# Kernel tuning notes

Measured on AMD Instinct MI355X. Metric: run time of the kernel, lower is better.

## Reference

```python
import jax, jax.numpy as jnp
import numpy as np

B, S, D, H = 4, 2048, 1024, 16
DEPTH = D // H
NEG = -1000000000.0


def setup_inputs() -> dict:
    key = jax.random.key(0)
    ks = jax.random.split(key, 11)
    scale = 1.0 / np.sqrt(D)
    return {
        "q": jax.random.normal(ks[0], (B, S, D), jnp.float32),
        "k": jax.random.normal(ks[1], (B, S, D), jnp.float32),
        "v": jax.random.normal(ks[2], (B, S, D), jnp.float32),
        "wq_w": jax.random.normal(ks[3], (D, D), jnp.float32) * scale,
        "wq_b": jax.random.normal(ks[4], (D,), jnp.float32) * 0.01,
        "wk_w": jax.random.normal(ks[5], (D, D), jnp.float32) * scale,
        "wk_b": jax.random.normal(ks[6], (D,), jnp.float32) * 0.01,
        "wv_w": jax.random.normal(ks[7], (D, D), jnp.float32) * scale,
        "wv_b": jax.random.normal(ks[8], (D,), jnp.float32) * 0.01,
        "dense_w": jax.random.normal(ks[9], (D, D), jnp.float32) * scale,
        "dense_b": jax.random.normal(ks[10], (D,), jnp.float32) * 0.01,
    }


def _split_heads(x):
    # (B, S, D) -> (B, H, S, depth)
    b, s, _ = x.shape
    return x.reshape(b, s, H, DEPTH).transpose(0, 2, 1, 3)


def reference(q, k, v, wq_w, wq_b, wk_w, wk_b, wv_w, wv_b, dense_w, dense_b):
    b, s, _ = q.shape
    qh = _split_heads(q @ wq_w.T + wq_b)
    kh = _split_heads(k @ wk_w.T + wk_b)
    vh = _split_heads(v @ wv_w.T + wv_b)
    logits = jnp.einsum('bhqd,bhkd->bhqk', qh, kh) / np.sqrt(DEPTH).astype(np.float32)
    # additive causal mask (strict upper triangle = -1e9)
    mask = jnp.where(jnp.triu(jnp.ones((s, s), jnp.float32), k=1) == 1.0, NEG, 0.0)
    logits = logits + mask
    attn = jax.nn.softmax(logits, axis=-1)
    out = jnp.einsum('bhqk,bhkd->bhqd', attn, vh)
    out = out.transpose(0, 2, 1, 3).reshape(b, s, D)
    return out @ dense_w.T + dense_b
```

## Files before the change

kernel.cpp:

```cpp
#include <hip/hip_runtime.h>
#include <hip/hip_bf16.h>


typedef __attribute__((ext_vector_type(8))) short bf16x8;
typedef __attribute__((ext_vector_type(4))) float f32x4;
typedef __attribute__((ext_vector_type(8))) unsigned short u16x8;

#define MFMA16(a, b, c) __builtin_amdgcn_mfma_f32_16x16x32_bf16(a, b, c, 0, 0, 0)

#define GLOAD_LDS16(gp, lp)                                                    \
  __builtin_amdgcn_global_load_lds(                                            \
      (const __attribute__((address_space(1))) void*)(gp),                     \
      (__attribute__((address_space(3))) void*)(lp), 16, 0, 0)

__device__ __forceinline__ unsigned short f2bf(float f) {
  union { float f; unsigned u; } x; x.f = f;
  unsigned u = x.u;
  return (unsigned short)((u + 0x7fffu + ((u >> 16) & 1u)) >> 16);
}

__device__ __forceinline__ unsigned pk2(float a, float b) {
  union { __hip_bfloat162 h; unsigned u; } cv;
  cv.h = __float22bfloat162_rn(float2{a, b});
  return cv.u;
}

__global__ __launch_bounds__(256) void convert_kernel(
    const float* __restrict__ q, const float* __restrict__ k,
    const float* __restrict__ v, const float* __restrict__ wq,
    const float* __restrict__ wk, const float* __restrict__ wv,
    const float* __restrict__ wd, const float* __restrict__ bq,
    const float* __restrict__ bk, const float* __restrict__ bv,
    unsigned short* __restrict__ dst, float* __restrict__ bias_pack) {
  const size_t tid0 = (size_t)blockIdx.x * blockDim.x + threadIdx.x;
  const size_t nthreads = (size_t)gridDim.x * blockDim.x;
  if (tid0 < 3072) {
    bias_pack[tid0] = tid0 < 1024 ? bq[tid0]
                     : (tid0 < 2048 ? bk[tid0 - 1024] : bv[tid0 - 2048]);
  }
  const size_t NQ = 8192ull * 1024;
  const size_t NW = 1024ull * 1024;
  const size_t total_chunks = (3 * NQ + 4 * NW) / 8;
  for (size_t c = tid0; c < total_chunks; c += nthreads) {
    const size_t e = c * 8;
    const float* src;
    if (e < NQ) src = q + e;
    else if (e < 2 * NQ) src = k + (e - NQ);
    else if (e < 3 * NQ) src = v + (e - 2 * NQ);
    else {
      const size_t we = e - 3 * NQ;
      if (we < NW) src = wq + we;
      else if (we < 2 * NW) src = wk + (we - NW);
      else if (we < 3 * NW) src = wv + (we - 2 * NW);
      else src = wd + (we - 3 * NW);
    }
    f32x4 a = *(const f32x4*)(src);
    f32x4 b = *(const f32x4*)(src + 4);
    u16x8 o;
    o[0] = f2bf(a[0]); o[1] = f2bf(a[1]); o[2] = f2bf(a[2]); o[3] = f2bf(a[3]);
    o[4] = f2bf(b[0]); o[5] = f2bf(b[1]); o[6] = f2bf(b[2]); o[7] = f2bf(b[3]);
    *(u16x8*)(dst + e) = o;
  }
}

template <int MODE>
__global__ __launch_bounds__(256) void gemm_kernel(
    const unsigned short* __restrict__ Abase,
    const unsigned short* __restrict__ Wbase,
    const float* __restrict__ biasbase, unsigned short* __restrict__ dstb,
    float* __restrict__ dstf) {
  __shared__ __attribute__((aligned(16))) unsigned short Ablk[128 * 32];
  __shared__ __attribute__((aligned(16))) unsigned short Bblk[128 * 32];
  const int z = blockIdx.z;
  const unsigned short* A = Abase + (size_t)z * (8192ull * 1024);
  const unsigned short* W = Wbase + (size_t)z * (1024ull * 1024);
  const float* bias = biasbase + (size_t)z * 1024;
  const int m0 = blockIdx.y * 128, n0 = blockIdx.x * 128;
  const int tid = threadIdx.x, lane = tid & 63, w = tid >> 6;
  const int wr = (w >> 1) * 64, wc = (w & 1) * 64;
  const int llo = lane & 15, lhi = lane >> 4;
  f32x4 acc[4][4] = {};
  const unsigned short* ag = A + (size_t)(m0 + (tid >> 2)) * 1024 + (tid & 3) * 8;
  const unsigned short* wg = W + (size_t)(n0 + (tid >> 2)) * 1024 + (tid & 3) * 8;
  unsigned short* lA = &Ablk[tid * 8];
  unsigned short* lA2 = &Ablk[2048 + tid * 8];
  unsigned short* lB = &Bblk[tid * 8];
  unsigned short* lB2 = &Bblk[2048 + tid * 8];
  for (int kt = 0; kt < 32; ++kt) {
    const int ko = kt * 32;
    if (kt) __syncthreads();
    GLOAD_LDS16(ag + ko, lA);
    GLOAD_LDS16(ag + ko + 64 * 1024, lA2);
    GLOAD_LDS16(wg + ko, lB);
    GLOAD_LDS16(wg + ko + 64 * 1024, lB2);
    __syncthreads();
    bf16x8 af[4], bfr[4];
#pragma unroll
    for (int i = 0; i < 4; ++i)
      af[i] = *(const bf16x8*)&Ablk[(wr + i * 16 + llo) * 32 + lhi * 8];
#pragma unroll
    for (int i = 0; i < 4; ++i)
      bfr[i] = *(const bf16x8*)&Bblk[(wc + i * 16 + llo) * 32 + lhi * 8];
#pragma unroll
    for (int mi = 0; mi < 4; ++mi)
#pragma unroll
      for (int ni = 0; ni < 4; ++ni)
        acc[mi][ni] = MFMA16(af[mi], bfr[ni], acc[mi][ni]);
  }
  const float osc = (MODE == 0 && z == 0) ? 0.1803368801f : 1.0f;
#pragma unroll
  for (int mi = 0; mi < 4; ++mi) {
#pragma unroll
    for (int ni = 0; ni < 4; ++ni) {
      const int n = n0 + wc + ni * 16 + llo;
      const float bv = (MODE == 2) ? 0.f : bias[n];
#pragma unroll
      for (int r = 0; r < 4; ++r) {
        const int m = m0 + wr + mi * 16 + lhi * 4 + r;
        float val = acc[mi][ni][r] + bv;
        if (MODE == 0) {
          val *= osc;
          const int b = m >> 11, s = m & 2047, h = n >> 6, d = n & 63;
          dstb[(size_t)z * (8192ull * 1024) +
               (((size_t)(b * 16 + h) * 2048 + s) * 64 + d)] = f2bf(val);
        } else if (MODE == 1) {
          dstf[(size_t)m * 1024 + n] = val;
        } else {
          val = acc[mi][ni][r] + bias[m];
          const int h = m >> 6, d = m & 63, b = n >> 11, sidx = n & 2047;
          const int t = sidx & 63;
          const int ps = (sidx & ~63) | ((t & 15) << 2) | (t >> 4);
          dstb[(((size_t)(b * 16 + h) * 64 + d) * 2048 + ps)] = f2bf(val);
        }
      }
    }
  }
}

__global__ __launch_bounds__(256, 4) void attn_kernel(
    const unsigned short* __restrict__ Qp, const unsigned short* __restrict__ Kp,
    const unsigned short* __restrict__ Vtp, unsigned short* __restrict__ attn_out) {
  __shared__ __attribute__((aligned(16))) unsigned short Klds[64 * 64];
  __shared__ __attribute__((aligned(16))) unsigned short Vt[80 * 64];
  __shared__ __attribute__((aligned(16))) unsigned short Plds[4 * 32 * 72];
  const int bh = blockIdx.x;
  const int qt = 15 - blockIdx.y;
  const int tid = threadIdx.x, lane = tid & 63, w = tid >> 6;
  const int llo = lane & 15, lhi = lane >> 4;
  const int q0 = qt * 128;
  const int qbase = q0 + w * 32;

  {
    const unsigned v16 = (tid < 16) ? 0x3F80u : 0u;
    const unsigned vv = v16 | (v16 << 16);
    *(uint2*)&Vt[64 * 64 + tid * 4] = make_uint2(vv, vv);
  }

  bf16x8 qf[2][2];
#pragma unroll
  for (int mi = 0; mi < 2; ++mi) {
    const unsigned short* qptr =
        Qp + ((size_t)bh * 2048 + qbase + mi * 16 + llo) * 64 + lhi * 8;
    qf[mi][0] = *(const bf16x8*)qptr;
    qf[mi][1] = *(const bf16x8*)(qptr + 32);
  }

  f32x4 o[2][5] = {};

  const size_t kbase = (size_t)bh * (64 * 2048);
  const int r0 = tid >> 3, r1 = r0 + 32;
  const int scb = (tid & 7) * 16;
  const int kcol0 = (scb ^ ((r0 & 7) << 4)) >> 1;
  const int kcol1 = (scb ^ ((r1 & 7) << 4)) >> 1;
  const int koff0 = r0 * 64 + kcol0, koff1 = r1 * 64 + kcol1;
  const int voff0 = r0 * 2048 + kcol0, voff1 = r1 * 2048 + kcol1;
  unsigned short* pw = &Plds[w * (32 * 72)];

  const int nkt = 2 * (qt + 1);
  for (int kt = 0; kt < nkt; ++kt) {
    const int kv0 = kt * 64;
    if (kt) __syncthreads();
    GLOAD_LDS16(Kp + kbase + (size_t)kv0 * 64 + koff0, &Klds[tid * 8]);
    GLOAD_LDS16(Kp + kbase + (size_t)kv0 * 64 + koff1, &Klds[2048 + tid * 8]);
    GLOAD_LDS16(Vtp + kbase + kv0 + voff0, &Vt[tid * 8]);
    GLOAD_LDS16(Vtp + kbase + kv0 + voff1, &Vt[2048 + tid * 8]);
    __syncthreads();
    if (kv0 > qbase + 31) continue;

    f32x4 s[2][4] = {};
#pragma unroll
    for (int b4 = 0; b4 < 4; ++b4) {
      const int row = b4 * 16 + llo;
      const int sw = (row & 7) << 3;
      const bf16x8 k0 = *(const bf16x8*)&Klds[row * 64 + ((lhi * 8) ^ sw)];
      const bf16x8 k1 = *(const bf16x8*)&Klds[row * 64 + ((32 + lhi * 8) ^ sw)];
      s[0][b4] = MFMA16(qf[0][0], k0, s[0][b4]);
      s[0][b4] = MFMA16(qf[0][1], k1, s[0][b4]);
      s[1][b4] = MFMA16(qf[1][0], k0, s[1][b4]);
      s[1][b4] = MFMA16(qf[1][1], k1, s[1][b4]);
    }

    const bool needm = (kv0 + 63 > qbase);
#pragma unroll
    for (int mi = 0; mi < 2; ++mi) {
#pragma unroll
      for (int r = 0; r < 4; ++r) {
        float sv0 = s[mi][0][r], sv1 = s[mi][1][r];
        float sv2 = s[mi][2][r], sv3 = s[mi][3][r];
        if (needm) {
          const int qrow = qbase + mi * 16 + lhi * 4 + r;
          if (kv0 + llo > qrow) sv0 = -1e9f;
          if (kv0 + 16 + llo > qrow) sv1 = -1e9f;
          if (kv0 + 32 + llo > qrow) sv2 = -1e9f;
          if (kv0 + 48 + llo > qrow) sv3 = -1e9f;
        }
        const float p0 = exp2f(sv0), p1 = exp2f(sv1);
        const float p2 = exp2f(sv2), p3 = exp2f(sv3);
        const int prow = mi * 16 + lhi * 4 + r;
        *(uint2*)&pw[prow * 72 + llo * 4] = make_uint2(pk2(p0, p1), pk2(p2, p3));
      }
    }

    bf16x8 pa[2][2];
#pragma unroll
    for (int mi = 0; mi < 2; ++mi) {
      pa[mi][0] = *(const bf16x8*)&pw[(mi * 16 + llo) * 72 + lhi * 8];
      pa[mi][1] = *(const bf16x8*)&pw[(mi * 16 + llo) * 72 + 32 + lhi * 8];
    }
#pragma unroll
    for (int dblk = 0; dblk < 5; ++dblk) {
      const int row = dblk * 16 + llo;
      const int sw = (row & 7) << 3;
      const bf16x8 v0 = *(const bf16x8*)&Vt[row * 64 + ((lhi * 8) ^ sw)];
      const bf16x8 v1 = *(const bf16x8*)&Vt[row * 64 + ((32 + lhi * 8) ^ sw)];
      o[0][dblk] = MFMA16(pa[0][0], v0, o[0][dblk]);
      o[0][dblk] = MFMA16(pa[0][1], v1, o[0][dblk]);
      o[1][dblk] = MFMA16(pa[1][0], v0, o[1][dblk]);
      o[1][dblk] = MFMA16(pa[1][1], v1, o[1][dblk]);
    }
  }

  const int b = bh >> 4, h = bh & 15;
#pragma unroll
  for (int mi = 0; mi < 2; ++mi) {
#pragma unroll
    for (int r = 0; r < 4; ++r) {
      const float lsum = __shfl(o[mi][4][r], lane & 48);
      const float inv = 1.0f / lsum;
      const int qrow = qbase + mi * 16 + lhi * 4 + r;
      const size_t base = ((size_t)b * 2048 + qrow) * 1024 + h * 64;
#pragma unroll
      for (int dblk = 0; dblk < 4; ++dblk)
        attn_out[base + dblk * 16 + llo] = f2bf(o[mi][dblk][r] * inv);
    }
  }
}

extern "C" void kernel_launch(void* const* d_in, const int* in_sizes, int n_in,
                              void* d_out, int out_size, void* d_ws,
                              size_t ws_size, hipStream_t stream) {
  const float* q = (const float*)d_in[0];
  const float* k = (const float*)d_in[1];
  const float* v = (const float*)d_in[2];
  const float* wq_w = (const float*)d_in[3];
  const float* wq_b = (const float*)d_in[4];
  const float* wk_w = (const float*)d_in[5];
  const float* wk_b = (const float*)d_in[6];
  const float* wv_w = (const float*)d_in[7];
  const float* wv_b = (const float*)d_in[8];
  const float* dense_w = (const float*)d_in[9];
  const float* dense_b = (const float*)d_in[10];
  float* out = (float*)d_out;

  char* ws = (char*)d_ws;
  const size_t MB = 1024ull * 1024;
  unsigned short* qkv_bf = (unsigned short*)(ws);
  unsigned short* w_bf = (unsigned short*)(ws + 48 * MB);
  float* bias_pack = (float*)(ws + 56 * MB);
  unsigned short* qkvp = (unsigned short*)(ws + 57 * MB);
  unsigned short* attn_o = (unsigned short*)(ws + 105 * MB);
  const size_t PEL = 8192ull * 1024;

  convert_kernel<<<dim3(2048), dim3(256), 0, stream>>>(
      q, k, v, wq_w, wk_w, wv_w, dense_w, wq_b, wk_b, wv_b, qkv_bf, bias_pack);

  gemm_kernel<0><<<dim3(8, 64, 2), dim3(256), 0, stream>>>(
      qkv_bf, w_bf, bias_pack, qkvp, nullptr);

  gemm_kernel<2><<<dim3(64, 8, 1), dim3(256), 0, stream>>>(
      w_bf + 2ull * 1024 * 1024, qkv_bf + 2 * PEL, bias_pack + 2048,
      qkvp + 2 * PEL, nullptr);

  attn_kernel<<<dim3(64, 16), dim3(256), 0, stream>>>(
      qkvp, qkvp + PEL, qkvp + 2 * PEL, attn_o);

  gemm_kernel<1><<<dim3(8, 64, 1), dim3(256), 0, stream>>>(
      attn_o, w_bf + 3ull * 1024 * 1024, dense_b, nullptr, out);
}
```

Measured before the change: 211.9 us.

## Merge V projection into QKV GEMM launch and read K/V directly from global in attention

```diff
diff --git a/kernel.cpp b/kernel.cpp
--- a/kernel.cpp
+++ b/kernel.cpp
@@ -71,11 +71,23 @@
     float* __restrict__ dstf) {
   __shared__ __attribute__((aligned(16))) unsigned short Ablk[128 * 32];
   __shared__ __attribute__((aligned(16))) unsigned short Bblk[128 * 32];
+  const size_t NQ = 8192ull * 1024, NW = 1024ull * 1024;
   const int z = blockIdx.z;
-  const unsigned short* A = Abase + (size_t)z * (8192ull * 1024);
-  const unsigned short* W = Wbase + (size_t)z * (1024ull * 1024);
+  const unsigned short* A;
+  const unsigned short* W;
+  int m0, n0;
+  if (MODE == 0 && z == 2) {
+    A = Wbase + 2 * NW;
+    W = Abase + 2 * NQ;
+    m0 = blockIdx.x * 128;
+    n0 = blockIdx.y * 128;
+  } else {
+    A = Abase + (size_t)z * NQ;
+    W = Wbase + (size_t)z * NW;
+    m0 = blockIdx.y * 128;
+    n0 = blockIdx.x * 128;
+  }
   const float* bias = biasbase + (size_t)z * 1024;
-  const int m0 = blockIdx.y * 128, n0 = blockIdx.x * 128;
   const int tid = threadIdx.x, lane = tid & 63, w = tid >> 6;
   const int wr = (w >> 1) * 64, wc = (w & 1) * 64;
   const int llo = lane & 15, lhi = lane >> 4;
@@ -113,24 +125,24 @@
 #pragma unroll
     for (int ni = 0; ni < 4; ++ni) {
       const int n = n0 + wc + ni * 16 + llo;
-      const float bv = (MODE == 2) ? 0.f : bias[n];
+      const float bv = (MODE == 0) ? ((z == 2) ? 0.f : bias[n]) : bias[n];
 #pragma unroll
       for (int r = 0; r < 4; ++r) {
         const int m = m0 + wr + mi * 16 + lhi * 4 + r;
         float val = acc[mi][ni][r] + bv;
-        if (MODE == 0) {
+        if (MODE == 1) {
+          dstf[(size_t)m * 1024 + n] = val;
+        } else if (z < 2) {
           val *= osc;
           const int b = m >> 11, s = m & 2047, h = n >> 6, d = n & 63;
-          dstb[(size_t)z * (8192ull * 1024) +
+          dstb[(size_t)z * NQ +
                (((size_t)(b * 16 + h) * 2048 + s) * 64 + d)] = f2bf(val);
-        } else if (MODE == 1) {
-          dstf[(size_t)m * 1024 + n] = val;
         } else {
           val = acc[mi][ni][r] + bias[m];
           const int h = m >> 6, d = m & 63, b = n >> 11, sidx = n & 2047;
           const int t = sidx & 63;
           const int ps = (sidx & ~63) | ((t & 15) << 2) | (t >> 4);
-          dstb[(((size_t)(b * 16 + h) * 64 + d) * 2048 + ps)] = f2bf(val);
+          dstb[2 * NQ + (((size_t)(b * 16 + h) * 64 + d) * 2048 + ps)] = f2bf(val);
         }
       }
     }
@@ -140,21 +152,12 @@
 __global__ __launch_bounds__(256, 4) void attn_kernel(
     const unsigned short* __restrict__ Qp, const unsigned short* __restrict__ Kp,
     const unsigned short* __restrict__ Vtp, unsigned short* __restrict__ attn_out) {
-  __shared__ __attribute__((aligned(16))) unsigned short Klds[64 * 64];
-  __shared__ __attribute__((aligned(16))) unsigned short Vt[80 * 64];
   __shared__ __attribute__((aligned(16))) unsigned short Plds[4 * 32 * 72];
   const int bh = blockIdx.x;
   const int qt = 15 - blockIdx.y;
   const int tid = threadIdx.x, lane = tid & 63, w = tid >> 6;
   const int llo = lane & 15, lhi = lane >> 4;
-  const int q0 = qt * 128;
-  const int qbase = q0 + w * 32;
-
-  {
-    const unsigned v16 = (tid < 16) ? 0x3F80u : 0u;
-    const unsigned vv = v16 | (v16 << 16);
-    *(uint2*)&Vt[64 * 64 + tid * 4] = make_uint2(vv, vv);
-  }
+  const int qbase = qt * 128 + w * 32;
 
   bf16x8 qf[2][2];
 #pragma unroll
@@ -165,40 +168,34 @@
     qf[mi][1] = *(const bf16x8*)(qptr + 32);
   }
 
+  bf16x8 ones;
+#pragma unroll
+  for (int i = 0; i < 8; ++i) ones[i] = (short)0x3F80;
+
   f32x4 o[2][5] = {};
 
   const size_t kbase = (size_t)bh * (64 * 2048);
-  const int r0 = tid >> 3, r1 = r0 + 32;
-  const int scb = (tid & 7) * 16;
-  const int kcol0 = (scb ^ ((r0 & 7) << 4)) >> 1;
-  const int kcol1 = (scb ^ ((r1 & 7) << 4)) >> 1;
-  const int koff0 = r0 * 64 + kcol0, koff1 = r1 * 64 + kcol1;
-  const int voff0 = r0 * 2048 + kcol0, voff1 = r1 * 2048 + kcol1;
+  const unsigned short* kfrag = Kp + kbase + (size_t)llo * 64 + lhi * 8;
+  const unsigned short* vfrag = Vtp + kbase + (size_t)llo * 2048 + lhi * 8;
   unsigned short* pw = &Plds[w * (32 * 72)];
 
-  const int nkt = 2 * (qt + 1);
+  const int nkt = (qbase + 31) / 64 + 1;
   for (int kt = 0; kt < nkt; ++kt) {
     const int kv0 = kt * 64;
-    if (kt) __syncthreads();
-    GLOAD_LDS16(Kp + kbase + (size_t)kv0 * 64 + koff0, &Klds[tid * 8]);
-    GLOAD_LDS16(Kp + kbase + (size_t)kv0 * 64 + koff1, &Klds[2048 + tid * 8]);
-    GLOAD_LDS16(Vtp + kbase + kv0 + voff0, &Vt[tid * 8]);
-    GLOAD_LDS16(Vtp + kbase + kv0 + voff1, &Vt[2048 + tid * 8]);
-    __syncthreads();
-    if (kv0 > qbase + 31) continue;
 
     f32x4 s[2][4] = {};
+    __builtin_amdgcn_s_setprio(1);
 #pragma unroll
     for (int b4 = 0; b4 < 4; ++b4) {
-      const int row = b4 * 16 + llo;
-      const int sw = (row & 7) << 3;
-      const bf16x8 k0 = *(const bf16x8*)&Klds[row * 64 + ((lhi * 8) ^ sw)];
-      const bf16x8 k1 = *(const bf16x8*)&Klds[row * 64 + ((32 + lhi * 8) ^ sw)];
+      const unsigned short* kp = kfrag + (size_t)(kv0 + b4 * 16) * 64;
+      const bf16x8 k0 = *(const bf16x8*)kp;
+      const bf16x8 k1 = *(const bf16x8*)(kp + 32);
       s[0][b4] = MFMA16(qf[0][0], k0, s[0][b4]);
       s[0][b4] = MFMA16(qf[0][1], k1, s[0][b4]);
       s[1][b4] = MFMA16(qf[1][0], k0, s[1][b4]);
       s[1][b4] = MFMA16(qf[1][1], k1, s[1][b4]);
     }
+    __builtin_amdgcn_s_setprio(0);
 
     const bool needm = (kv0 + 63 > qbase);
 #pragma unroll
@@ -227,17 +224,22 @@
       pa[mi][0] = *(const bf16x8*)&pw[(mi * 16 + llo) * 72 + lhi * 8];
       pa[mi][1] = *(const bf16x8*)&pw[(mi * 16 + llo) * 72 + 32 + lhi * 8];
     }
-#pragma unroll
-    for (int dblk = 0; dblk < 5; ++dblk) {
-      const int row = dblk * 16 + llo;
-      const int sw = (row & 7) << 3;
-      const bf16x8 v0 = *(const bf16x8*)&Vt[row * 64 + ((lhi * 8) ^ sw)];
-      const bf16x8 v1 = *(const bf16x8*)&Vt[row * 64 + ((32 + lhi * 8) ^ sw)];
+    __builtin_amdgcn_s_setprio(1);
+#pragma unroll
+    for (int dblk = 0; dblk < 4; ++dblk) {
+      const unsigned short* vp = vfrag + (size_t)(dblk * 16) * 2048 + kv0;
+      const bf16x8 v0 = *(const bf16x8*)vp;
+      const bf16x8 v1 = *(const bf16x8*)(vp + 32);
       o[0][dblk] = MFMA16(pa[0][0], v0, o[0][dblk]);
       o[0][dblk] = MFMA16(pa[0][1], v1, o[0][dblk]);
       o[1][dblk] = MFMA16(pa[1][0], v0, o[1][dblk]);
       o[1][dblk] = MFMA16(pa[1][1], v1, o[1][dblk]);
     }
+    o[0][4] = MFMA16(pa[0][0], ones, o[0][4]);
+    o[0][4] = MFMA16(pa[0][1], ones, o[0][4]);
+    o[1][4] = MFMA16(pa[1][0], ones, o[1][4]);
+    o[1][4] = MFMA16(pa[1][1], ones, o[1][4]);
+    __builtin_amdgcn_s_setprio(0);
   }
 
   const int b = bh >> 4, h = bh & 15;
@@ -245,8 +247,7 @@
   for (int mi = 0; mi < 2; ++mi) {
 #pragma unroll
     for (int r = 0; r < 4; ++r) {
-      const float lsum = __shfl(o[mi][4][r], lane & 48);
-      const float inv = 1.0f / lsum;
+      const float inv = 1.0f / o[mi][4][r];
       const int qrow = qbase + mi * 16 + lhi * 4 + r;
       const size_t base = ((size_t)b * 2048 + qrow) * 1024 + h * 64;
 #pragma unroll
@@ -284,12 +285,8 @@
   convert_kernel<<<dim3(2048), dim3(256), 0, stream>>>(
       q, k, v, wq_w, wk_w, wv_w, dense_w, wq_b, wk_b, wv_b, qkv_bf, bias_pack);
 
-  gemm_kernel<0><<<dim3(8, 64, 2), dim3(256), 0, stream>>>(
+  gemm_kernel<0><<<dim3(8, 64, 3), dim3(256), 0, stream>>>(
       qkv_bf, w_bf, bias_pack, qkvp, nullptr);
-
-  gemm_kernel<2><<<dim3(64, 8, 1), dim3(256), 0, stream>>>(
-      w_bf + 2ull * 1024 * 1024, qkv_bf + 2 * PEL, bias_pack + 2048,
-      qkvp + 2 * PEL, nullptr);
 
   attn_kernel<<<dim3(64, 16), dim3(256), 0, stream>>>(
       qkvp, qkvp + PEL, qkvp + 2 * PEL, attn_o);
```

Result: slower. 294.5 us (+39.0%).
